# Kernel tuning notes

Measured on AMD Instinct MI355X. Metric: run time of the kernel, lower is better.

The kernel has to match this reference:

```python
import jax, jax.numpy as jnp
import numpy as np

GRID = 128          # fine voxel grid extent
N_PTS = 300000
C = 64              # hidden channels


def _encode(c, B):
    c = c.astype(np.int64)
    return (c[:, 0] * B + c[:, 1]) * B + c[:, 2]


def _kernel_map(in_coords, out_coords, offsets, n_out):
    """ME-style kernel map: for each kernel offset, (input_idx, output_idx) pairs
    where in_coord == out_coord + offset. Padded to a fixed length with a dummy
    output row n_out (sliced off later)."""
    B = GRID * 4
    keys = _encode(in_coords + 4, B)           # +4 shift keeps keys nonneg
    order = np.argsort(keys)
    skeys = keys[order]
    ins, outs = [], []
    for off in offsets:
        q = _encode(out_coords + 4 + off, B)
        pos = np.clip(np.searchsorted(skeys, q), 0, len(skeys) - 1)
        valid = skeys[pos] == q
        ins.append(order[pos[valid]].astype(np.int32))
        outs.append(np.nonzero(valid)[0].astype(np.int32))
    L = max(len(a) for a in ins)
    K = len(offsets)
    in_idx = np.zeros((K, L), np.int32)
    out_idx = np.full((K, L), n_out, np.int32)   # pad -> dummy row
    for k in range(K):
        m = len(ins[k])
        in_idx[k, :m] = ins[k]
        out_idx[k, :m] = outs[k]
    return in_idx, out_idx


def setup_inputs() -> dict:
    rng = np.random.default_rng(0)
    flat = rng.choice(GRID ** 3, size=N_PTS, replace=False)
    coords = np.stack(np.unravel_index(flat, (GRID,) * 3), axis=1).astype(np.int64)
    u = np.unique(coords // 2, axis=0)           # stride-2 output coords (coarse units)
    n2 = u.shape[0]

    r = np.arange(-1, 2)
    off27 = np.stack(np.meshgrid(r, r, r, indexing='ij'), -1).reshape(-1, 3)
    r2 = np.arange(0, 2)
    off8 = np.stack(np.meshgrid(r2, r2, r2, indexing='ij'), -1).reshape(-1, 3)

    map1_in, map1_out = _kernel_map(coords, coords, off27, N_PTS)   # k=3, s=1
    map2_in, map2_out = _kernel_map(coords, 2 * u, off8, n2)        # k=2, s=2
    map3_in, map3_out = _kernel_map(u, u, off27, n2)                # k=3, s=1 on coarse lattice

    key = jax.random.key(0)
    ks = jax.random.split(key, 8)
    sc1 = 1.0 / np.sqrt(27 * 8)
    sc2 = 1.0 / np.sqrt(8 * C)
    sc3 = 1.0 / np.sqrt(27 * C)
    return {
        'feats': jax.random.normal(ks[0], (N_PTS, 8), jnp.float32),
        'W1': jax.random.normal(ks[1], (27, 8, C), jnp.float32) * sc1,
        'b1': jax.random.normal(ks[2], (C,), jnp.float32) * 0.01,
        'W2': jax.random.normal(ks[3], (8, C, C), jnp.float32) * sc2,
        'b2': jax.random.normal(ks[4], (C,), jnp.float32) * 0.01,
        'W3': jax.random.normal(ks[5], (27, C, 8), jnp.float32) * sc3,
        'b3': jax.random.normal(ks[6], (8,), jnp.float32) * 0.01,
        'map1_in': jnp.asarray(map1_in), 'map1_out': jnp.asarray(map1_out),
        'map2_in': jnp.asarray(map2_in), 'map2_out': jnp.asarray(map2_out),
        'map3_in': jnp.asarray(map3_in), 'map3_out': jnp.asarray(map3_out),
        'n2': int(n2),
    }


def _sparse_conv(x, W, b, in_idx, out_idx, n_out):
    # gather-GEMM-scatter over K kernel offsets; padded pairs land on dummy row n_out
    y = jnp.zeros((n_out + 1, W.shape[-1]), x.dtype)
    for k in range(W.shape[0]):
        y = y.at[out_idx[k]].add(x[in_idx[k]] @ W[k])
    return y[:n_out] + b


def reference(feats, W1, b1, W2, b2, W3, b3,
              map1_in, map1_out, map2_in, map2_out, map3_in, map3_out, n2):
    n1 = feats.shape[0]
    h = jax.nn.relu(_sparse_conv(feats, W1, b1, map1_in, map1_out, n1))
    h = jax.nn.relu(_sparse_conv(h, W2, b2, map2_in, map2_out, n2))
    return _sparse_conv(h, W3, b3, map3_in, map3_out, n2)
```

## Files before the change

### kernel.cpp

```cpp
#include <hip/hip_runtime.h>


#define TPB 256

__device__ __forceinline__ int xcd_chunk(int bid, int nwg) {
  int q = nwg >> 3, r = nwg & 7;
  int xcd = bid & 7, idx = bid >> 3;
  int base = (xcd < r) ? xcd * (q + 1) : r * (q + 1) + (xcd - r) * q;
  return base + idx;
}

__global__ void __launch_bounds__(TPB)
k_build(const int* __restrict__ mi, const int* __restrict__ mo,
        int* __restrict__ tbl, int L, int n_out) {
  int k = blockIdx.y;
  int p = blockIdx.x * TPB + threadIdx.x;
  if (p >= L) return;
  int out = mo[(size_t)k * L + p];
  bool valid = out < n_out;
  if (__ballot(valid) == 0ull) return;
  if (valid) tbl[(size_t)k * n_out + out] = mi[(size_t)k * L + p];
}

__global__ void __launch_bounds__(TPB)
k_conv1(const float* __restrict__ x, const float* __restrict__ W1,
        const float* __restrict__ b1, const int* __restrict__ t1,
        float* __restrict__ h1, int n1) {
  int r = blockIdx.x * TPB + threadIdx.x;
  if (r >= n1) return;
  int j0 = blockIdx.y * 32;
  float acc[32];
#pragma unroll
  for (int j = 0; j < 32; ++j) acc[j] = 0.f;
#pragma unroll 1
  for (int k = 0; k < 27; ++k) {
    int idx = t1[(size_t)k * n1 + r];
    bool v = idx >= 0;
    if (__ballot(v) == 0ull) continue;
    const float4* xr = (const float4*)(x + (size_t)(v ? idx : 0) * 8);
    float4 a = xr[0], b = xr[1];
    if (!v) { a = make_float4(0.f,0.f,0.f,0.f); b = make_float4(0.f,0.f,0.f,0.f); }
    float xv[8] = {a.x, a.y, a.z, a.w, b.x, b.y, b.z, b.w};
    const float* __restrict__ Wk = W1 + (size_t)k * 512 + j0;
#pragma unroll
    for (int i = 0; i < 8; ++i)
#pragma unroll
      for (int j = 0; j < 32; ++j)
        acc[j] = fmaf(xv[i], Wk[i * 64 + j], acc[j]);
  }
  float4* yr = (float4*)(h1 + (size_t)r * 64 + j0);
#pragma unroll
  for (int q = 0; q < 8; ++q) {
    float4 o;
    o.x = fmaxf(acc[4*q+0] + b1[j0+4*q+0], 0.f);
    o.y = fmaxf(acc[4*q+1] + b1[j0+4*q+1], 0.f);
    o.z = fmaxf(acc[4*q+2] + b1[j0+4*q+2], 0.f);
    o.w = fmaxf(acc[4*q+3] + b1[j0+4*q+3], 0.f);
    yr[q] = o;
  }
}

__global__ void __launch_bounds__(TPB)
k_conv2(const float* __restrict__ h1, const float* __restrict__ W2,
        const float* __restrict__ b2, const int* __restrict__ t2,
        float* __restrict__ h2, int n1, int n2, int nwg) {
  int b = xcd_chunk(blockIdx.x, nwg);
  int jq = b & 3, xb = b >> 2;
  int r = xb * TPB + threadIdx.x;
  if (r >= n2) return;
  int j0 = jq * 16;
  float acc[16];
#pragma unroll
  for (int j = 0; j < 16; ++j) acc[j] = 0.f;
#pragma unroll 1
  for (int k = 0; k < 8; ++k) {
    int idx = t2[(size_t)k * n2 + r];
    int row = idx >= 0 ? idx : n1;
    const float4* xr = (const float4*)(h1 + (size_t)row * 64);
    const float* __restrict__ Wk = W2 + (size_t)k * 4096 + j0;
#pragma unroll 4
    for (int c = 0; c < 16; ++c) {
      float4 xv = xr[c];
#pragma unroll
      for (int j = 0; j < 16; ++j) {
        acc[j] = fmaf(xv.x, Wk[(4*c+0)*64 + j], acc[j]);
        acc[j] = fmaf(xv.y, Wk[(4*c+1)*64 + j], acc[j]);
        acc[j] = fmaf(xv.z, Wk[(4*c+2)*64 + j], acc[j]);
        acc[j] = fmaf(xv.w, Wk[(4*c+3)*64 + j], acc[j]);
      }
    }
  }
  float4* yr = (float4*)(h2 + (size_t)r * 64 + j0);
#pragma unroll
  for (int q = 0; q < 4; ++q) {
    float4 o;
    o.x = fmaxf(acc[4*q+0] + b2[j0+4*q+0], 0.f);
    o.y = fmaxf(acc[4*q+1] + b2[j0+4*q+1], 0.f);
    o.z = fmaxf(acc[4*q+2] + b2[j0+4*q+2], 0.f);
    o.w = fmaxf(acc[4*q+3] + b2[j0+4*q+3], 0.f);
    yr[q] = o;
  }
}

__global__ void __launch_bounds__(TPB)
k_conv3(const float* __restrict__ h2, const float* __restrict__ W3,
        const float* __restrict__ b3, const int* __restrict__ t3,
        float* __restrict__ out, int n2, int nwg) {
  __shared__ float red[4][64][9];
  int b = xcd_chunk(blockIdx.x, nwg);
  int w = __builtin_amdgcn_readfirstlane(threadIdx.x >> 6);
  int l = threadIdx.x & 63;
  int r = b * 64 + l;
  int rc = r < n2 ? r : n2 - 1;
  float acc[8];
#pragma unroll
  for (int j = 0; j < 8; ++j) acc[j] = 0.f;
  int nk = (w < 3) ? 7 : 6;
  int idx = t3[(size_t)w * n2 + rc];
#pragma unroll 1
  for (int i = 0; i < nk; ++i) {
    int k = w + 4 * i;
    int row = idx >= 0 ? idx : n2;
    if (i + 1 < nk) idx = t3[(size_t)(k + 4) * n2 + rc];
    const float4* xr = (const float4*)(h2 + (size_t)row * 64);
    const float* __restrict__ Wk = W3 + (size_t)k * 512;
#pragma unroll
    for (int c = 0; c < 16; ++c) {
      float4 xv = xr[c];
      float hv[4] = {xv.x, xv.y, xv.z, xv.w};
#pragma unroll
      for (int u = 0; u < 4; ++u)
#pragma unroll
        for (int j = 0; j < 8; ++j)
          acc[j] = fmaf(hv[u], Wk[(4*c+u)*8 + j], acc[j]);
    }
  }
#pragma unroll
  for (int j = 0; j < 8; ++j) red[w][l][j] = acc[j];
  __syncthreads();
#pragma unroll
  for (int t = threadIdx.x; t < 512; t += TPB) {
    int row = t >> 3, ch = t & 7;
    int g = b * 64 + row;
    if (g < n2) {
      float s = red[0][row][ch] + red[1][row][ch]
              + red[2][row][ch] + red[3][row][ch];
      out[(size_t)g * 8 + ch] = s + b3[ch];
    }
  }
}

extern "C" void kernel_launch(void* const* d_in, const int* in_sizes, int n_in,
                              void* d_out, int out_size, void* d_ws, size_t ws_size,
                              hipStream_t stream) {
  const float* feats = (const float*)d_in[0];
  const float* W1 = (const float*)d_in[1];
  const float* b1 = (const float*)d_in[2];
  const float* W2 = (const float*)d_in[3];
  const float* b2 = (const float*)d_in[4];
  const float* W3 = (const float*)d_in[5];
  const float* b3 = (const float*)d_in[6];
  const int* m1i = (const int*)d_in[7];
  const int* m1o = (const int*)d_in[8];
  const int* m2i = (const int*)d_in[9];
  const int* m2o = (const int*)d_in[10];
  const int* m3i = (const int*)d_in[11];
  const int* m3o = (const int*)d_in[12];

  int n1 = in_sizes[0] / 8;
  int L1 = in_sizes[7] / 27;
  int L2 = in_sizes[9] / 8;
  int L3 = in_sizes[11] / 27;
  int n2 = out_size / 8;

  char* ws = (char*)d_ws;
  size_t y1_bytes = (size_t)(n1 + 1) * 64 * sizeof(float);
  size_t y2_bytes = (size_t)(n2 + 1) * 64 * sizeof(float);
  size_t t1_bytes = (size_t)27 * n1 * sizeof(int);
  size_t reg1_bytes = y2_bytes > t1_bytes ? y2_bytes : t1_bytes;
  float* y1 = (float*)ws;
  float* y2 = (float*)(ws + y1_bytes);
  int* t1 = (int*)(ws + y1_bytes);
  int* t2 = (int*)(ws + y1_bytes + reg1_bytes);
  int* t3 = (int*)(ws + y1_bytes + reg1_bytes + (size_t)8 * n2 * sizeof(int));

  hipMemsetAsync(t1, 0xFF, t1_bytes, stream);
  hipMemsetAsync(t2, 0xFF, (size_t)8 * n2 * sizeof(int), stream);
  hipMemsetAsync(t3, 0xFF, (size_t)27 * n2 * sizeof(int), stream);

  k_build<<<dim3((L1 + TPB - 1) / TPB, 27), TPB, 0, stream>>>(m1i, m1o, t1, L1, n1);
  k_build<<<dim3((L2 + TPB - 1) / TPB, 8), TPB, 0, stream>>>(m2i, m2o, t2, L2, n2);
  k_build<<<dim3((L3 + TPB - 1) / TPB, 27), TPB, 0, stream>>>(m3i, m3o, t3, L3, n2);

  k_conv1<<<dim3((n1 + TPB - 1) / TPB, 2), TPB, 0, stream>>>(feats, W1, b1, t1, y1, n1);

  hipMemsetAsync(y1 + (size_t)n1 * 64, 0, 64 * sizeof(float), stream);
  hipMemsetAsync(y2 + (size_t)n2 * 64, 0, 64 * sizeof(float), stream);

  int nb2 = ((n2 + TPB - 1) / TPB) * 4;
  k_conv2<<<nb2, TPB, 0, stream>>>(y1, W2, b2, t2, y2, n1, n2, nb2);

  int nb3 = (n2 + 63) / 64;
  k_conv3<<<nb3, TPB, 0, stream>>>(y2, W3, b3, t3, (float*)d_out, n2, nb3);
}
```

Before: 600.8 us.

## Transpose conv1 neighbor table to row-major and map one wave per output row

The conv1 neighbor table now has one padded row of 28 entries per output point instead of one plane per kernel offset, so a wave can read all of a row's neighbor indices with vector loads. Conv1 is restructured so each 64-lane wave computes one output row, with each lane producing one channel, and loops over two rows. The aim is coalesced h1 writes, uniform per-row skipping of missing neighbors, and less register pressure than the previous 32-accumulator-per-thread layout. The cost is that every lane loads the same feature row and the build kernel's table writes become scattered across rows.

New measurement: 2.155 ms. 259% more time.

```diff
diff --git a/kernel.cpp b/kernel.cpp
--- a/kernel.cpp
+++ b/kernel.cpp
@@ -23,40 +23,50 @@
 }
 
 __global__ void __launch_bounds__(TPB)
+k_build1(const int* __restrict__ mi, const int* __restrict__ mo,
+         int* __restrict__ tbl, int L, int n1) {
+  int k = blockIdx.y;
+  int p = blockIdx.x * TPB + threadIdx.x;
+  if (p >= L) return;
+  int out = mo[(size_t)k * L + p];
+  bool valid = out < n1;
+  if (__ballot(valid) == 0ull) return;
+  if (valid) tbl[(size_t)out * 28 + k] = mi[(size_t)k * L + p];
+}
+
+__global__ void __launch_bounds__(TPB)
 k_conv1(const float* __restrict__ x, const float* __restrict__ W1,
         const float* __restrict__ b1, const int* __restrict__ t1,
         float* __restrict__ h1, int n1) {
-  int r = blockIdx.x * TPB + threadIdx.x;
-  if (r >= n1) return;
-  int j0 = blockIdx.y * 32;
-  float acc[32];
-#pragma unroll
-  for (int j = 0; j < 32; ++j) acc[j] = 0.f;
+  int wgl = blockIdx.x * 4 + (threadIdx.x >> 6);
+  int j = threadIdx.x & 63;
+  float b1v = b1[j];
 #pragma unroll 1
-  for (int k = 0; k < 27; ++k) {
-    int idx = t1[(size_t)k * n1 + r];
-    bool v = idx >= 0;
-    if (__ballot(v) == 0ull) continue;
-    const float4* xr = (const float4*)(x + (size_t)(v ? idx : 0) * 8);
-    float4 a = xr[0], b = xr[1];
-    if (!v) { a = make_float4(0.f,0.f,0.f,0.f); b = make_float4(0.f,0.f,0.f,0.f); }
-    float xv[8] = {a.x, a.y, a.z, a.w, b.x, b.y, b.z, b.w};
-    const float* __restrict__ Wk = W1 + (size_t)k * 512 + j0;
-#pragma unroll
-    for (int i = 0; i < 8; ++i)
-#pragma unroll
-      for (int j = 0; j < 32; ++j)
-        acc[j] = fmaf(xv[i], Wk[i * 64 + j], acc[j]);
-  }
-  float4* yr = (float4*)(h1 + (size_t)r * 64 + j0);
-#pragma unroll
-  for (int q = 0; q < 8; ++q) {
-    float4 o;
-    o.x = fmaxf(acc[4*q+0] + b1[j0+4*q+0], 0.f);
-    o.y = fmaxf(acc[4*q+1] + b1[j0+4*q+1], 0.f);
-    o.z = fmaxf(acc[4*q+2] + b1[j0+4*q+2], 0.f);
-    o.w = fmaxf(acc[4*q+3] + b1[j0+4*q+3], 0.f);
-    yr[q] = o;
+  for (int rr = 0; rr < 2; ++rr) {
+    int r = __builtin_amdgcn_readfirstlane(wgl * 2 + rr);
+    if (r >= n1) return;
+    const int4* trow = (const int4*)(t1 + (size_t)r * 28);
+    int idxs[28];
+#pragma unroll
+    for (int q = 0; q < 7; ++q) *(int4*)&idxs[4 * q] = trow[q];
+    float acc = 0.f;
+#pragma unroll
+    for (int k = 0; k < 27; ++k) {
+      int idx = idxs[k];
+      if (idx < 0) continue;
+      const float4* xs = (const float4*)(x + (size_t)idx * 8);
+      float4 xa = xs[0], xb = xs[1];
+      const float* __restrict__ Wc = W1 + k * 512 + j;
+      acc = fmaf(xa.x, Wc[0 * 64], acc);
+      acc = fmaf(xa.y, Wc[1 * 64], acc);
+      acc = fmaf(xa.z, Wc[2 * 64], acc);
+      acc = fmaf(xa.w, Wc[3 * 64], acc);
+      acc = fmaf(xb.x, Wc[4 * 64], acc);
+      acc = fmaf(xb.y, Wc[5 * 64], acc);
+      acc = fmaf(xb.z, Wc[6 * 64], acc);
+      acc = fmaf(xb.w, Wc[7 * 64], acc);
+    }
+    h1[(size_t)r * 64 + j] = fmaxf(acc + b1v, 0.f);
   }
 }
 
@@ -176,7 +186,7 @@
   char* ws = (char*)d_ws;
   size_t y1_bytes = (size_t)(n1 + 1) * 64 * sizeof(float);
   size_t y2_bytes = (size_t)(n2 + 1) * 64 * sizeof(float);
-  size_t t1_bytes = (size_t)27 * n1 * sizeof(int);
+  size_t t1_bytes = (size_t)n1 * 28 * sizeof(int);
   size_t reg1_bytes = y2_bytes > t1_bytes ? y2_bytes : t1_bytes;
   float* y1 = (float*)ws;
   float* y2 = (float*)(ws + y1_bytes);
@@ -188,11 +198,12 @@
   hipMemsetAsync(t2, 0xFF, (size_t)8 * n2 * sizeof(int), stream);
   hipMemsetAsync(t3, 0xFF, (size_t)27 * n2 * sizeof(int), stream);
 
-  k_build<<<dim3((L1 + TPB - 1) / TPB, 27), TPB, 0, stream>>>(m1i, m1o, t1, L1, n1);
+  k_build1<<<dim3((L1 + TPB - 1) / TPB, 27), TPB, 0, stream>>>(m1i, m1o, t1, L1, n1);
   k_build<<<dim3((L2 + TPB - 1) / TPB, 8), TPB, 0, stream>>>(m2i, m2o, t2, L2, n2);
   k_build<<<dim3((L3 + TPB - 1) / TPB, 27), TPB, 0, stream>>>(m3i, m3o, t3, L3, n2);
 
-  k_conv1<<<dim3((n1 + TPB - 1) / TPB, 2), TPB, 0, stream>>>(feats, W1, b1, t1, y1, n1);
+  int nwaves1 = (n1 + 1) / 2;
+  k_conv1<<<(nwaves1 + 3) / 4, TPB, 0, stream>>>(feats, W1, b1, t1, y1, n1);
 
   hipMemsetAsync(y1 + (size_t)n1 * 64, 0, 64 * sizeof(float), stream);
   hipMemsetAsync(y2 + (size_t)n2 * 64, 0, 64 * sizeof(float), stream);
```
